# Kernel optimization log

Measured on AMD Instinct MI355X. Metric: run time of the kernel, lower is better.

Reference implementation:

```python
import jax, jax.numpy as jnp
import numpy as np

BS, NC, BH, BW, C = 1, 6, 100, 100, 256
HG, WG = 100, 40
HF, WF = 48, 80
HEADS, PTS, HD = 8, 8, 32
MAXOV = 2
NQ = HG * WG


def _nearest_sample(img, grid):
    # img: [B,H,W,Ch], grid: [B,Hg,Wg,2] in [-1,1]; nearest, align_corners=True, zeros padding
    B, H, W, _ = img.shape
    ix = jnp.round((grid[..., 0] + 1.0) * 0.5 * (W - 1))
    iy = jnp.round((grid[..., 1] + 1.0) * 0.5 * (H - 1))
    valid = (ix >= 0) & (ix <= W - 1) & (iy >= 0) & (iy <= H - 1)
    xc = jnp.clip(ix, 0, W - 1).astype(jnp.int32)
    yc = jnp.clip(iy, 0, H - 1).astype(jnp.int32)
    b = jnp.arange(B)[:, None, None]
    return img[b, yc, xc] * valid[..., None]


def _bilinear_sample(img, x, y):
    # img: [B,H,W,Ch]; x,y: [B,N] unnormalized (align_corners=False); zeros padding
    B, H, W, _ = img.shape
    x0 = jnp.floor(x)
    y0 = jnp.floor(y)
    wx1 = x - x0
    wy1 = y - y0
    b = jnp.arange(B)[:, None]

    def corner(xi, yi):
        valid = (xi >= 0) & (xi <= W - 1) & (yi >= 0) & (yi <= H - 1)
        xc = jnp.clip(xi, 0, W - 1).astype(jnp.int32)
        yc = jnp.clip(yi, 0, H - 1).astype(jnp.int32)
        return img[b, yc, xc] * valid[..., None]

    return (corner(x0, y0) * ((1 - wx1) * (1 - wy1))[..., None]
            + corner(x0 + 1, y0) * (wx1 * (1 - wy1))[..., None]
            + corner(x0, y0 + 1) * ((1 - wx1) * wy1)[..., None]
            + corner(x0 + 1, y0 + 1) * (wx1 * wy1)[..., None])


def _forward(query, value, queries_rebatch_grid, restore_bev_grid,
             reference_points_rebatch, bev_pillar_counts, query_pos,
             Wv, bv, Woff, boff, Watt, batt, Wout, bout, spatial_shapes):
    inp_residual = query
    q = query + query_pos                                       # [BS, BH*BW, C]
    # --- rebatch BEV queries per camera via nearest grid_sample ---
    qmap = jnp.broadcast_to(q.reshape(BS, 1, BH, BW, C),
                            (BS, NC, BH, BW, C)).reshape(BS * NC, BH, BW, C)
    q_reb = _nearest_sample(qmap, queries_rebatch_grid).reshape(BS * NC, NQ, C)
    ref = reference_points_rebatch.reshape(BS * NC, NQ, 2)      # flatten(-2): [BNC,NQ,2,1]->[BNC,NQ,2]
    # --- value projection ---
    v = value.transpose(2, 0, 1, 3).reshape(BS * NC, HF * WF, C)
    v = (v @ Wv + bv).reshape(BS * NC, HF, WF, HEADS, HD)
    # --- multi-scale deformable attention (single level) ---
    off = (q_reb @ Woff + boff).reshape(BS * NC, NQ, HEADS, PTS, 2)
    attw = jax.nn.softmax((q_reb @ Watt + batt).reshape(BS * NC, NQ, HEADS, PTS), axis=-1)
    normalizer = jnp.flip(spatial_shapes[0], 0).astype(jnp.float32)  # [WF, HF]
    loc = ref[:, :, None, None, :] + off / normalizer           # [BNC,NQ,HEADS,PTS,2] in [0,1]
    x = (loc[..., 0] * WF - 0.5).transpose(0, 2, 1, 3).reshape(BS * NC * HEADS, NQ * PTS)
    y = (loc[..., 1] * HF - 0.5).transpose(0, 2, 1, 3).reshape(BS * NC * HEADS, NQ * PTS)
    vh = v.transpose(0, 3, 1, 2, 4).reshape(BS * NC * HEADS, HF, WF, HD)
    samp = _bilinear_sample(vh, x, y).reshape(BS * NC, HEADS, NQ, PTS, HD)
    out = jnp.einsum('bhnpd,bnhp->bnhd', samp, attw).reshape(BS * NC, NQ, C)
    queries_out = out.transpose(0, 2, 1)                        # [BNC, C, NQ] (channels-first as module expects)
    # --- restore to BEV feature ---
    qo = queries_out.reshape(BS, NC, C, NQ).transpose(0, 2, 1, 3).reshape(BS, C, NC * HG, WG)
    bevq = _nearest_sample(qo.transpose(0, 2, 3, 1), restore_bev_grid)  # [BS, MAXOV*BH, BW, C]
    bevq = bevq.transpose(0, 3, 1, 2)                           # [BS, C, MAXOV*BH, BW]
    # reshape(BS, C*MAXOV, BH, BW) + all-ones grouped 1x1 conv == sum of the two overlap copies
    slots = bevq[:, :, :BH, :] + bevq[:, :, BH:, :]             # [BS, C, BH, BW]
    slots = slots.reshape(BS, C, BH * BW).transpose(0, 2, 1)    # [BS, BH*BW, C]
    slots = slots * bev_pillar_counts
    slots = slots @ Wout + bout
    return slots + inp_residual  # dropout identity in eval


def setup_inputs():
    key = jax.random.key(0)
    ks = jax.random.split(key, 14)
    s = 1.0 / np.sqrt(C)
    return {
        "query": jax.random.normal(ks[0], (BS, BH * BW, C), jnp.float32),
        "value": jax.random.normal(ks[1], (BS, HF * WF, NC, C), jnp.float32),
        "queries_rebatch_grid": jax.random.uniform(ks[2], (BS * NC, HG, WG, 2), jnp.float32, -1.0, 1.0),
        "restore_bev_grid": jax.random.uniform(ks[3], (BS, MAXOV * BH, BW, 2), jnp.float32, -1.0, 1.0),
        "reference_points_rebatch": jax.random.uniform(ks[4], (BS * NC, NQ, 2, 1), jnp.float32),
        "bev_pillar_counts": jax.random.uniform(ks[5], (BS, BH * BW, 1), jnp.float32),
        "query_pos": jax.random.normal(ks[6], (BS, BH * BW, C), jnp.float32),
        "Wv": jax.random.uniform(ks[7], (C, C), jnp.float32, -s, s),
        "bv": jnp.zeros((C,), jnp.float32),
        "Woff": jax.random.normal(ks[8], (C, HEADS * PTS * 2), jnp.float32) * 0.01,
        "boff": jax.random.uniform(ks[9], (HEADS * PTS * 2,), jnp.float32, -2.0, 2.0),
        "Watt": jax.random.normal(ks[10], (C, HEADS * PTS), jnp.float32) * 0.01,
        "batt": jnp.zeros((HEADS * PTS,), jnp.float32),
        "Wout": jax.random.uniform(ks[11], (C, C), jnp.float32, -s, s),
        "bout": jnp.zeros((C,), jnp.float32),
        "spatial_shapes": jnp.array([[HF, WF]], dtype=jnp.int32),
    }


def reference(query, value, queries_rebatch_grid, restore_bev_grid,
              reference_points_rebatch, bev_pillar_counts, query_pos,
              Wv, bv, Woff, boff, Watt, batt, Wout, bout, spatial_shapes):
    return _forward(query, value, queries_rebatch_grid, restore_bev_grid,
                    reference_points_rebatch, bev_pillar_counts, query_pos,
                    Wv, bv, Woff, boff, Watt, batt, Wout, bout, spatial_shapes)
```

## Files before the change

kernel.cpp:

```cpp
#include <hip/hip_runtime.h>
#include <hip/hip_bf16.h>
#include <math.h>

#define NCAMS 6
#define BH_ 100
#define BW_ 100
#define CDIM 256
#define NQ_ 4000
#define HF_ 48
#define WF_ 80
#define HEADS_ 8
#define PTS_ 8
#define HD_ 32
#define HWV (HF_*WF_)
#define M1_ (NCAMS*HWV)
#define M2_ (NCAMS*NQ_)
#define NOUT_ 10000

#define SA 264

typedef __bf16 bf16_t;
typedef __bf16 bf16x8 __attribute__((ext_vector_type(8)));
typedef __bf16 bf16x4 __attribute__((ext_vector_type(4)));
typedef float  f32x4  __attribute__((ext_vector_type(4)));

static __device__ __forceinline__ f32x4 mfma16(bf16x8 a, bf16x8 b, f32x4 c) {
    return __builtin_amdgcn_mfma_f32_16x16x32_bf16(a, b, c, 0, 0, 0);
}

__global__ __launch_bounds__(256) void k0_prep(const float* __restrict__ Wv,
                                               const float* __restrict__ Woff,
                                               const float* __restrict__ Watt,
                                               const float* __restrict__ Wout,
                                               bf16_t* __restrict__ WvT,
                                               bf16_t* __restrict__ WcombT,
                                               bf16_t* __restrict__ WoutT) {
    int b = blockIdx.x, k = threadIdx.x;
    if (b < 256) {
        WvT[b * 256 + k] = (bf16_t)Wv[k * 256 + b];
    } else if (b < 448) {
        int n = b - 256;
        float v = (n < 128) ? Woff[k * 128 + n] : Watt[k * 64 + (n - 128)];
        WcombT[n * 256 + k] = (bf16_t)v;
    } else {
        int n = b - 448;
        WoutT[n * 256 + k] = (bf16_t)Wout[k * 256 + n];
    }
}

__global__ __launch_bounds__(256) void k1_vproj(const float* __restrict__ value,
                                                const bf16_t* __restrict__ WvT,
                                                const float* __restrict__ bv,
                                                bf16_t* __restrict__ vh) {
    __shared__ __align__(16) bf16_t At[32 * SA];
    const int m0 = blockIdx.x * 32;
    const int cam = m0 / HWV;
    const int hw0 = m0 - cam * HWV;
    for (int idx = threadIdx.x; idx < 32 * 64; idx += 256) {
        int r = idx >> 6, c4 = idx & 63;
        float4 v = ((const float4*)value)[((hw0 + r) * NCAMS + cam) * 64 + c4];
        bf16x4 pk; pk[0] = (bf16_t)v.x; pk[1] = (bf16_t)v.y; pk[2] = (bf16_t)v.z; pk[3] = (bf16_t)v.w;
        *(bf16x4*)(At + r * SA + c4 * 4) = pk;
    }
    __syncthreads();
    const int lane = threadIdx.x & 63, w = threadIdx.x >> 6;
    const int lr = lane & 15, lk = lane >> 4;
    f32x4 acc[2][4] = {};
    const bf16_t* a0 = At + lr * SA + lk * 8;
    const bf16_t* b0 = WvT + (w * 64 + lr) * 256 + lk * 8;
#pragma unroll
    for (int ks = 0; ks < 8; ++ks) {
        bf16x8 af[2], bf_[4];
#pragma unroll
        for (int m = 0; m < 2; ++m) af[m] = *(const bf16x8*)(a0 + m * 16 * SA + ks * 32);
#pragma unroll
        for (int n = 0; n < 4; ++n) bf_[n] = *(const bf16x8*)(b0 + n * 16 * 256 + ks * 32);
#pragma unroll
        for (int m = 0; m < 2; ++m)
#pragma unroll
            for (int n = 0; n < 4; ++n)
                acc[m][n] = mfma16(af[m], bf_[n], acc[m][n]);
    }
    __syncthreads();
#pragma unroll
    for (int n = 0; n < 4; ++n) {
        int col = w * 64 + n * 16 + lr;
        float bias = bv[col];
#pragma unroll
        for (int m = 0; m < 2; ++m)
#pragma unroll
            for (int j = 0; j < 4; ++j)
                At[(m * 16 + lk * 4 + j) * SA + col] = (bf16_t)(acc[m][n][j] + bias);
    }
    __syncthreads();
    for (int idx = threadIdx.x; idx < 32 * 32; idx += 256) {
        int r = idx >> 5, g = idx & 31;
        int head = g >> 2, part = g & 3;
        bf16x8 v = *(const bf16x8*)(At + r * SA + g * 8);
        *(bf16x8*)(vh + ((size_t)(cam * HEADS_ + head) * HWV + hw0 + r) * HD_ + part * 8) = v;
    }
}

__global__ __launch_bounds__(256) void k2_offatt(const float* __restrict__ query,
                                                 const float* __restrict__ qpos,
                                                 const float* __restrict__ qgrid,
                                                 const bf16_t* __restrict__ WcombT,
                                                 const float* __restrict__ boff,
                                                 const float* __restrict__ batt,
                                                 float* __restrict__ off_ws,
                                                 float* __restrict__ att_ws) {
    __shared__ __align__(16) bf16_t At[32 * SA];
    __shared__ int rowpos[32];
    const int m0 = blockIdx.x * 32;
    if (threadIdx.x < 32) {
        int m = m0 + threadIdx.x;
        float gx = qgrid[m * 2 + 0], gy = qgrid[m * 2 + 1];
        float fx = rintf(__fmul_rn(__fmul_rn(__fadd_rn(gx, 1.0f), 0.5f), 99.0f));
        float fy = rintf(__fmul_rn(__fmul_rn(__fadd_rn(gy, 1.0f), 0.5f), 99.0f));
        bool valid = (fx >= 0.0f) && (fx <= 99.0f) && (fy >= 0.0f) && (fy <= 99.0f);
        rowpos[threadIdx.x] = valid ? ((int)fy * BW_ + (int)fx) : -1;
    }
    __syncthreads();
    const float4* q4 = (const float4*)query;
    const float4* p4 = (const float4*)qpos;
    for (int idx = threadIdx.x; idx < 32 * 64; idx += 256) {
        int r = idx >> 6, c4 = idx & 63;
        int p = rowpos[r];
        bf16x4 pk;
        if (p >= 0) {
            float4 a = q4[p * 64 + c4];
            float4 b = p4[p * 64 + c4];
            pk[0] = (bf16_t)(a.x + b.x); pk[1] = (bf16_t)(a.y + b.y);
            pk[2] = (bf16_t)(a.z + b.z); pk[3] = (bf16_t)(a.w + b.w);
        } else {
            pk[0] = (bf16_t)0.0f; pk[1] = (bf16_t)0.0f; pk[2] = (bf16_t)0.0f; pk[3] = (bf16_t)0.0f;
        }
        *(bf16x4*)(At + r * SA + c4 * 4) = pk;
    }
    __syncthreads();
    const int lane = threadIdx.x & 63, w = threadIdx.x >> 6;
    const int lr = lane & 15, lk = lane >> 4;
    const int wcol0 = w * 48;
    f32x4 acc[2][3] = {};
    const bf16_t* a0 = At + lr * SA + lk * 8;
    const bf16_t* b0 = WcombT + (wcol0 + lr) * 256 + lk * 8;
#pragma unroll
    for (int ks = 0; ks < 8; ++ks) {
        bf16x8 af[2], bf_[3];
#pragma unroll
        for (int m = 0; m < 2; ++m) af[m] = *(const bf16x8*)(a0 + m * 16 * SA + ks * 32);
#pragma unroll
        for (int n = 0; n < 3; ++n) bf_[n] = *(const bf16x8*)(b0 + n * 16 * 256 + ks * 32);
#pragma unroll
        for (int m = 0; m < 2; ++m)
#pragma unroll
            for (int n = 0; n < 3; ++n)
                acc[m][n] = mfma16(af[m], bf_[n], acc[m][n]);
    }
#pragma unroll
    for (int n = 0; n < 3; ++n) {
        const int colbase = wcol0 + n * 16;
        const int col = colbase + lr;
        if (colbase < 128) {
            float bo = boff[col];
#pragma unroll
            for (int m = 0; m < 2; ++m)
#pragma unroll
                for (int j = 0; j < 4; ++j)
                    off_ws[(m0 + m * 16 + lk * 4 + j) * 128 + col] = acc[m][n][j] + bo;
        } else {
            float bt = batt[col - 128];
#pragma unroll
            for (int m = 0; m < 2; ++m)
#pragma unroll
                for (int j = 0; j < 4; ++j) {
                    float lg = acc[m][n][j] + bt;
                    float mx = lg;
                    mx = fmaxf(mx, __shfl_xor(mx, 1, 64));
                    mx = fmaxf(mx, __shfl_xor(mx, 2, 64));
                    mx = fmaxf(mx, __shfl_xor(mx, 4, 64));
                    float e = expf(lg - mx);
                    float s = e;
                    s += __shfl_xor(s, 1, 64);
                    s += __shfl_xor(s, 2, 64);
                    s += __shfl_xor(s, 4, 64);
                    att_ws[(m0 + m * 16 + lk * 4 + j) * 64 + (col - 128)] = e / s;
                }
        }
    }
}

__global__ __launch_bounds__(256) void k3_sample(const bf16_t* __restrict__ vh,
                                                 const float* __restrict__ refp,
                                                 const float* __restrict__ off_ws,
                                                 const float* __restrict__ att_ws,
                                                 bf16_t* __restrict__ out_attn) {
    const int lb = (blockIdx.x & 7) * 375 + (blockIdx.x >> 3);
    const int t = lb * 256 + threadIdx.x;
    const int u = t >> 2;
    const int j = t & 3;
    const int m = u >> 3;
    const int h = u & 7;
    const int cam = m / NQ_;
    const float rx = refp[m * 2 + 0];
    const float ry = refp[m * 2 + 1];
    const bf16_t* base = vh + (size_t)(cam * HEADS_ + h) * HWV * HD_ + j * 8;
    const float4* off4 = (const float4*)(off_ws + m * 128 + h * 16);
    const float4* att4 = (const float4*)(att_ws + m * 64 + h * 8);
    float4 o0 = off4[0], o1 = off4[1], o2 = off4[2], o3 = off4[3];
    float4 a0 = att4[0], a1 = att4[1];
    float offv[16] = {o0.x, o0.y, o0.z, o0.w, o1.x, o1.y, o1.z, o1.w,
                      o2.x, o2.y, o2.z, o2.w, o3.x, o3.y, o3.z, o3.w};
    float attv[8] = {a0.x, a0.y, a0.z, a0.w, a1.x, a1.y, a1.z, a1.w};
    float acc[8] = {};
#pragma unroll
    for (int p = 0; p < PTS_; ++p) {
        float ax = fmaf(rx, (float)WF_, offv[p * 2 + 0] - 0.5f);
        float ay = fmaf(ry, (float)HF_, offv[p * 2 + 1] - 0.5f);
        float x0f = floorf(ax), y0f = floorf(ay);
        float wx = ax - x0f, wy = ay - y0f;
        float att = attv[p];
        bool vx0 = (x0f >= 0.0f) && (x0f <= (float)(WF_ - 1));
        bool vx1 = (x0f >= -1.0f) && (x0f <= (float)(WF_ - 2));
        bool vy0 = (y0f >= 0.0f) && (y0f <= (float)(HF_ - 1));
        bool vy1 = (y0f >= -1.0f) && (y0f <= (float)(HF_ - 2));
        float aw00 = (vx0 && vy0) ? att * (1.0f - wx) * (1.0f - wy) : 0.0f;
        float aw01 = (vx1 && vy0) ? att * wx * (1.0f - wy) : 0.0f;
        float aw10 = (vx0 && vy1) ? att * (1.0f - wx) * wy : 0.0f;
        float aw11 = (vx1 && vy1) ? att * wx * wy : 0.0f;
        int x0 = (int)fminf(fmaxf(x0f, 0.0f), (float)(WF_ - 1));
        int x1 = (int)fminf(fmaxf(x0f + 1.0f, 0.0f), (float)(WF_ - 1));
        int y0 = (int)fminf(fmaxf(y0f, 0.0f), (float)(HF_ - 1));
        int y1 = (int)fminf(fmaxf(y0f + 1.0f, 0.0f), (float)(HF_ - 1));
        bf16x8 c00 = *(const bf16x8*)(base + (y0 * WF_ + x0) * HD_);
        bf16x8 c01 = *(const bf16x8*)(base + (y0 * WF_ + x1) * HD_);
        bf16x8 c10 = *(const bf16x8*)(base + (y1 * WF_ + x0) * HD_);
        bf16x8 c11 = *(const bf16x8*)(base + (y1 * WF_ + x1) * HD_);
#pragma unroll
        for (int c = 0; c < 8; ++c) {
            acc[c] = fmaf(aw00, (float)c00[c],
                     fmaf(aw01, (float)c01[c],
                     fmaf(aw10, (float)c10[c],
                     fmaf(aw11, (float)c11[c], acc[c]))));
        }
    }
    bf16x8 ov;
#pragma unroll
    for (int c = 0; c < 8; ++c) ov[c] = (bf16_t)acc[c];
    *(bf16x8*)(out_attn + (size_t)m * CDIM + h * HD_ + j * 8) = ov;
}

__global__ __launch_bounds__(256) void k4_restore(const bf16_t* __restrict__ out_attn,
                                                  const float* __restrict__ rgrid,
                                                  const float* __restrict__ counts,
                                                  const bf16_t* __restrict__ WoutT,
                                                  const float* __restrict__ bout,
                                                  const float* __restrict__ query,
                                                  float* __restrict__ out) {
    __shared__ __align__(16) bf16_t At[32 * SA];
    __shared__ int pos2[32][2];
    __shared__ float cnt[32];
    const int m0 = blockIdx.x * 32;
    if (threadIdx.x < 64) {
        int r = threadIdx.x >> 1, k = threadIdx.x & 1;
        int i = m0 + r;
        if (i < NOUT_) {
            int bh = i / 100, bw = i - bh * 100;
            int R = bh + k * BH_;
            float gx = rgrid[(R * 100 + bw) * 2 + 0], gy = rgrid[(R * 100 + bw) * 2 + 1];
            float fx = rintf(__fmul_rn(__fmul_rn(__fadd_rn(gx, 1.0f), 0.5f), 39.0f));
            float fy = rintf(__fmul_rn(__fmul_rn(__fadd_rn(gy, 1.0f), 0.5f), 599.0f));
            bool valid = (fx >= 0.0f) && (fx <= 39.0f) && (fy >= 0.0f) && (fy <= 599.0f);
            int ix = (int)fx, iy = (int)fy;
            int camr = iy / 100, hg = iy - camr * 100;
            pos2[r][k] = valid ? (camr * NQ_ + hg * 40 + ix) : -1;
            if (k == 0) cnt[r] = counts[i];
        } else {
            pos2[r][k] = -1;
            if (k == 0) cnt[r] = 0.0f;
        }
    }
    __syncthreads();
    for (int idx = threadIdx.x; idx < 32 * 32; idx += 256) {
        int r = idx >> 5, g = idx & 31;
        int p0 = pos2[r][0], p1 = pos2[r][1];
        float s[8] = {};
        if (p0 >= 0) {
            bf16x8 a = *(const bf16x8*)(out_attn + (size_t)p0 * CDIM + g * 8);
#pragma unroll
            for (int c = 0; c < 8; ++c) s[c] += (float)a[c];
        }
        if (p1 >= 0) {
            bf16x8 a = *(const bf16x8*)(out_attn + (size_t)p1 * CDIM + g * 8);
#pragma unroll
            for (int c = 0; c < 8; ++c) s[c] += (float)a[c];
        }
        float cn = cnt[r];
        bf16x8 pk;
#pragma unroll
        for (int c = 0; c < 8; ++c) pk[c] = (bf16_t)(s[c] * cn);
        *(bf16x8*)(At + r * SA + g * 8) = pk;
    }
    __syncthreads();
    const int lane = threadIdx.x & 63, w = threadIdx.x >> 6;
    const int lr = lane & 15, lk = lane >> 4;
    f32x4 acc[2][4] = {};
    const bf16_t* a0 = At + lr * SA + lk * 8;
    const bf16_t* b0 = WoutT + (w * 64 + lr) * 256 + lk * 8;
#pragma unroll
    for (int ks = 0; ks < 8; ++ks) {
        bf16x8 af[2], bf_[4];
#pragma unroll
        for (int m = 0; m < 2; ++m) af[m] = *(const bf16x8*)(a0 + m * 16 * SA + ks * 32);
#pragma unroll
        for (int n = 0; n < 4; ++n) bf_[n] = *(const bf16x8*)(b0 + n * 16 * 256 + ks * 32);
#pragma unroll
        for (int m = 0; m < 2; ++m)
#pragma unroll
            for (int n = 0; n < 4; ++n)
                acc[m][n] = mfma16(af[m], bf_[n], acc[m][n]);
    }
#pragma unroll
    for (int n = 0; n < 4; ++n) {
        int col = w * 64 + n * 16 + lr;
        float bo = bout[col];
#pragma unroll
        for (int m = 0; m < 2; ++m)
#pragma unroll
            for (int j = 0; j < 4; ++j) {
                int row = m0 + m * 16 + lk * 4 + j;
                if (row < NOUT_)
                    out[row * CDIM + col] = acc[m][n][j] + bo + query[row * CDIM + col];
            }
    }
}

extern "C" void kernel_launch(void* const* d_in, const int* in_sizes, int n_in,
                              void* d_out, int out_size, void* d_ws, size_t ws_size,
                              hipStream_t stream) {
    (void)in_sizes; (void)n_in; (void)out_size; (void)ws_size;
    const float* query  = (const float*)d_in[0];
    const float* value  = (const float*)d_in[1];
    const float* qgrid  = (const float*)d_in[2];
    const float* rgrid  = (const float*)d_in[3];
    const float* refp   = (const float*)d_in[4];
    const float* counts = (const float*)d_in[5];
    const float* qpos   = (const float*)d_in[6];
    const float* Wv     = (const float*)d_in[7];
    const float* bv     = (const float*)d_in[8];
    const float* Woff   = (const float*)d_in[9];
    const float* boff   = (const float*)d_in[10];
    const float* Watt   = (const float*)d_in[11];
    const float* batt   = (const float*)d_in[12];
    const float* Wout   = (const float*)d_in[13];
    const float* bout   = (const float*)d_in[14];
    float* out = (float*)d_out;
    char* w8 = (char*)d_ws;

    bf16_t* vh       = (bf16_t*)(w8);
    bf16_t* out_attn = (bf16_t*)(w8 + 11796480);
    float* off_ws    = (float*)(w8 + 24084480);
    float* att_ws    = (float*)(w8 + 36372480);
    bf16_t* WvT      = (bf16_t*)(w8 + 42516480);
    bf16_t* WcombT   = (bf16_t*)(w8 + 42647552);
    bf16_t* WoutT    = (bf16_t*)(w8 + 42745856);

    hipLaunchKernelGGL(k0_prep,   dim3(704),      dim3(256), 0, stream, Wv, Woff, Watt, Wout,
                       WvT, WcombT, WoutT);
    hipLaunchKernelGGL(k1_vproj,  dim3(M1_ / 32), dim3(256), 0, stream, value, WvT, bv, vh);
    hipLaunchKernelGGL(k2_offatt, dim3(M2_ / 32), dim3(256), 0, stream, query, qpos, qgrid,
                       WcombT, boff, batt, off_ws, att_ws);
    hipLaunchKernelGGL(k3_sample, dim3(3000),     dim3(256), 0, stream, vh, refp, off_ws,
                       att_ws, out_attn);
    hipLaunchKernelGGL(k4_restore, dim3(313),     dim3(256), 0, stream, out_attn, rgrid, counts,
                       WoutT, bout, query, out);
}
```

Measured before the change: 97.65 us.

## Fuse offset/attention projection with deformable sampling, keeping offsets in LDS

Merges the offset/attention GEMM kernel and the bilinear sampling kernel into one kernel. Each block handles 16 query rows, writes offsets and softmaxed attention weights to shared memory instead of global workspace, then samples the value map directly. This removes a launch and the global round trip of about 18 MB of fp32 offsets and weights. In exchange the GEMM tile shrinks to 16 rows, so each block reloads weight fragments for half as much work, and the block index is remapped so that consecutive row tiles stay on the same XCD.

Result: faster. 95.25 us (-2.5%).

```diff
diff --git a/kernel.cpp b/kernel.cpp
--- a/kernel.cpp
+++ b/kernel.cpp
@@ -18,6 +18,8 @@
 #define NOUT_ 10000
 
 #define SA 264
+#define SOFF 132
+#define SATT 68
 
 typedef __bf16 bf16_t;
 typedef __bf16 bf16x8 __attribute__((ext_vector_type(8)));
@@ -72,14 +74,14 @@
     for (int ks = 0; ks < 8; ++ks) {
         bf16x8 af[2], bf_[4];
 #pragma unroll
-        for (int m = 0; m < 2; ++m) af[m] = *(const bf16x8*)(a0 + m * 16 * SA + ks * 32);
+        for (int mm = 0; mm < 2; ++mm) af[mm] = *(const bf16x8*)(a0 + mm * 16 * SA + ks * 32);
 #pragma unroll
         for (int n = 0; n < 4; ++n) bf_[n] = *(const bf16x8*)(b0 + n * 16 * 256 + ks * 32);
 #pragma unroll
-        for (int m = 0; m < 2; ++m)
+        for (int mm = 0; mm < 2; ++mm)
 #pragma unroll
             for (int n = 0; n < 4; ++n)
-                acc[m][n] = mfma16(af[m], bf_[n], acc[m][n]);
+                acc[mm][n] = mfma16(af[mm], bf_[n], acc[mm][n]);
     }
     __syncthreads();
 #pragma unroll
@@ -87,10 +89,10 @@
         int col = w * 64 + n * 16 + lr;
         float bias = bv[col];
 #pragma unroll
-        for (int m = 0; m < 2; ++m)
+        for (int mm = 0; mm < 2; ++mm)
 #pragma unroll
             for (int j = 0; j < 4; ++j)
-                At[(m * 16 + lk * 4 + j) * SA + col] = (bf16_t)(acc[m][n][j] + bias);
+                At[(mm * 16 + lk * 4 + j) * SA + col] = (bf16_t)(acc[mm][n][j] + bias);
     }
     __syncthreads();
     for (int idx = threadIdx.x; idx < 32 * 32; idx += 256) {
@@ -101,153 +103,163 @@
     }
 }
 
-__global__ __launch_bounds__(256) void k2_offatt(const float* __restrict__ query,
-                                                 const float* __restrict__ qpos,
-                                                 const float* __restrict__ qgrid,
-                                                 const bf16_t* __restrict__ WcombT,
-                                                 const float* __restrict__ boff,
-                                                 const float* __restrict__ batt,
-                                                 float* __restrict__ off_ws,
-                                                 float* __restrict__ att_ws) {
-    __shared__ __align__(16) bf16_t At[32 * SA];
-    __shared__ int rowpos[32];
-    const int m0 = blockIdx.x * 32;
-    if (threadIdx.x < 32) {
+__global__ __launch_bounds__(256) void k23_offatt_sample(
+        const float* __restrict__ query,
+        const float* __restrict__ qpos,
+        const float* __restrict__ qgrid,
+        const bf16_t* __restrict__ WcombT,
+        const float* __restrict__ boff,
+        const float* __restrict__ batt,
+        const float* __restrict__ refp,
+        const bf16_t* __restrict__ vh,
+        bf16_t* __restrict__ out_attn) {
+    __shared__ __align__(16) char u_lds[16 * SOFF * 4 + 16 * SATT * 4];
+    bf16_t* At   = (bf16_t*)u_lds;
+    float*  offs = (float*)u_lds;
+    float*  atts = (float*)(u_lds + 16 * SOFF * 4);
+    __shared__ int rowpos[16];
+    __shared__ float rref[16][2];
+
+    const int orig = blockIdx.x;
+    const int xcd = orig & 7, idx8 = orig >> 3;
+    const int lb = (xcd < 4 ? xcd * 188 : 4 * 188 + (xcd - 4) * 187) + idx8;
+    const int m0 = lb * 16;
+    const int cam = m0 / NQ_;
+
+    if (threadIdx.x < 16) {
         int m = m0 + threadIdx.x;
         float gx = qgrid[m * 2 + 0], gy = qgrid[m * 2 + 1];
         float fx = rintf(__fmul_rn(__fmul_rn(__fadd_rn(gx, 1.0f), 0.5f), 99.0f));
         float fy = rintf(__fmul_rn(__fmul_rn(__fadd_rn(gy, 1.0f), 0.5f), 99.0f));
         bool valid = (fx >= 0.0f) && (fx <= 99.0f) && (fy >= 0.0f) && (fy <= 99.0f);
         rowpos[threadIdx.x] = valid ? ((int)fy * BW_ + (int)fx) : -1;
+    } else if (threadIdx.x < 48) {
+        int t = threadIdx.x - 16;
+        rref[t >> 1][t & 1] = refp[(m0 + (t >> 1)) * 2 + (t & 1)];
     }
     __syncthreads();
     const float4* q4 = (const float4*)query;
     const float4* p4 = (const float4*)qpos;
-    for (int idx = threadIdx.x; idx < 32 * 64; idx += 256) {
-        int r = idx >> 6, c4 = idx & 63;
-        int p = rowpos[r];
-        bf16x4 pk;
-        if (p >= 0) {
-            float4 a = q4[p * 64 + c4];
-            float4 b = p4[p * 64 + c4];
-            pk[0] = (bf16_t)(a.x + b.x); pk[1] = (bf16_t)(a.y + b.y);
-            pk[2] = (bf16_t)(a.z + b.z); pk[3] = (bf16_t)(a.w + b.w);
-        } else {
-            pk[0] = (bf16_t)0.0f; pk[1] = (bf16_t)0.0f; pk[2] = (bf16_t)0.0f; pk[3] = (bf16_t)0.0f;
-        }
-        *(bf16x4*)(At + r * SA + c4 * 4) = pk;
+    {
+        int idx = threadIdx.x;
+#pragma unroll
+        for (int it = 0; it < 4; ++it, idx += 256) {
+            int r = idx >> 6, c4 = idx & 63;
+            int p = rowpos[r];
+            bf16x4 pk;
+            if (p >= 0) {
+                float4 a = q4[p * 64 + c4];
+                float4 b = p4[p * 64 + c4];
+                pk[0] = (bf16_t)(a.x + b.x); pk[1] = (bf16_t)(a.y + b.y);
+                pk[2] = (bf16_t)(a.z + b.z); pk[3] = (bf16_t)(a.w + b.w);
+            } else {
+                pk[0] = (bf16_t)0.0f; pk[1] = (bf16_t)0.0f; pk[2] = (bf16_t)0.0f; pk[3] = (bf16_t)0.0f;
+            }
+            *(bf16x4*)(At + r * SA + c4 * 4) = pk;
+        }
     }
     __syncthreads();
     const int lane = threadIdx.x & 63, w = threadIdx.x >> 6;
     const int lr = lane & 15, lk = lane >> 4;
     const int wcol0 = w * 48;
-    f32x4 acc[2][3] = {};
-    const bf16_t* a0 = At + lr * SA + lk * 8;
-    const bf16_t* b0 = WcombT + (wcol0 + lr) * 256 + lk * 8;
-#pragma unroll
-    for (int ks = 0; ks < 8; ++ks) {
-        bf16x8 af[2], bf_[3];
-#pragma unroll
-        for (int m = 0; m < 2; ++m) af[m] = *(const bf16x8*)(a0 + m * 16 * SA + ks * 32);
-#pragma unroll
-        for (int n = 0; n < 3; ++n) bf_[n] = *(const bf16x8*)(b0 + n * 16 * 256 + ks * 32);
-#pragma unroll
-        for (int m = 0; m < 2; ++m)
+    f32x4 acc[3] = {};
+    {
+        const bf16_t* a0 = At + lr * SA + lk * 8;
+        const bf16_t* b0 = WcombT + (wcol0 + lr) * 256 + lk * 8;
+#pragma unroll
+        for (int ks = 0; ks < 8; ++ks) {
+            bf16x8 af = *(const bf16x8*)(a0 + ks * 32);
+            bf16x8 bf_[3];
+#pragma unroll
+            for (int n = 0; n < 3; ++n) bf_[n] = *(const bf16x8*)(b0 + n * 16 * 256 + ks * 32);
 #pragma unroll
             for (int n = 0; n < 3; ++n)
-                acc[m][n] = mfma16(af[m], bf_[n], acc[m][n]);
-    }
+                acc[n] = mfma16(af, bf_[n], acc[n]);
+        }
+    }
+    __syncthreads();
 #pragma unroll
     for (int n = 0; n < 3; ++n) {
         const int colbase = wcol0 + n * 16;
         const int col = colbase + lr;
+        const int rloc = lk * 4;
         if (colbase < 128) {
             float bo = boff[col];
 #pragma unroll
-            for (int m = 0; m < 2; ++m)
-#pragma unroll
-                for (int j = 0; j < 4; ++j)
-                    off_ws[(m0 + m * 16 + lk * 4 + j) * 128 + col] = acc[m][n][j] + bo;
+            for (int j = 0; j < 4; ++j)
+                offs[(rloc + j) * SOFF + col] = acc[n][j] + bo;
         } else {
             float bt = batt[col - 128];
 #pragma unroll
-            for (int m = 0; m < 2; ++m)
-#pragma unroll
-                for (int j = 0; j < 4; ++j) {
-                    float lg = acc[m][n][j] + bt;
-                    float mx = lg;
-                    mx = fmaxf(mx, __shfl_xor(mx, 1, 64));
-                    mx = fmaxf(mx, __shfl_xor(mx, 2, 64));
-                    mx = fmaxf(mx, __shfl_xor(mx, 4, 64));
-                    float e = expf(lg - mx);
-                    float s = e;
-                    s += __shfl_xor(s, 1, 64);
-                    s += __shfl_xor(s, 2, 64);
-                    s += __shfl_xor(s, 4, 64);
-                    att_ws[(m0 + m * 16 + lk * 4 + j) * 64 + (col - 128)] = e / s;
-                }
-        }
-    }
-}
-
-__global__ __launch_bounds__(256) void k3_sample(const bf16_t* __restrict__ vh,
-                                                 const float* __restrict__ refp,
-                                                 const float* __restrict__ off_ws,
-                                                 const float* __restrict__ att_ws,
-                                                 bf16_t* __restrict__ out_attn) {
-    const int lb = (blockIdx.x & 7) * 375 + (blockIdx.x >> 3);
-    const int t = lb * 256 + threadIdx.x;
-    const int u = t >> 2;
-    const int j = t & 3;
-    const int m = u >> 3;
-    const int h = u & 7;
-    const int cam = m / NQ_;
-    const float rx = refp[m * 2 + 0];
-    const float ry = refp[m * 2 + 1];
-    const bf16_t* base = vh + (size_t)(cam * HEADS_ + h) * HWV * HD_ + j * 8;
-    const float4* off4 = (const float4*)(off_ws + m * 128 + h * 16);
-    const float4* att4 = (const float4*)(att_ws + m * 64 + h * 8);
-    float4 o0 = off4[0], o1 = off4[1], o2 = off4[2], o3 = off4[3];
-    float4 a0 = att4[0], a1 = att4[1];
-    float offv[16] = {o0.x, o0.y, o0.z, o0.w, o1.x, o1.y, o1.z, o1.w,
-                      o2.x, o2.y, o2.z, o2.w, o3.x, o3.y, o3.z, o3.w};
-    float attv[8] = {a0.x, a0.y, a0.z, a0.w, a1.x, a1.y, a1.z, a1.w};
-    float acc[8] = {};
-#pragma unroll
-    for (int p = 0; p < PTS_; ++p) {
-        float ax = fmaf(rx, (float)WF_, offv[p * 2 + 0] - 0.5f);
-        float ay = fmaf(ry, (float)HF_, offv[p * 2 + 1] - 0.5f);
-        float x0f = floorf(ax), y0f = floorf(ay);
-        float wx = ax - x0f, wy = ay - y0f;
-        float att = attv[p];
-        bool vx0 = (x0f >= 0.0f) && (x0f <= (float)(WF_ - 1));
-        bool vx1 = (x0f >= -1.0f) && (x0f <= (float)(WF_ - 2));
-        bool vy0 = (y0f >= 0.0f) && (y0f <= (float)(HF_ - 1));
-        bool vy1 = (y0f >= -1.0f) && (y0f <= (float)(HF_ - 2));
-        float aw00 = (vx0 && vy0) ? att * (1.0f - wx) * (1.0f - wy) : 0.0f;
-        float aw01 = (vx1 && vy0) ? att * wx * (1.0f - wy) : 0.0f;
-        float aw10 = (vx0 && vy1) ? att * (1.0f - wx) * wy : 0.0f;
-        float aw11 = (vx1 && vy1) ? att * wx * wy : 0.0f;
-        int x0 = (int)fminf(fmaxf(x0f, 0.0f), (float)(WF_ - 1));
-        int x1 = (int)fminf(fmaxf(x0f + 1.0f, 0.0f), (float)(WF_ - 1));
-        int y0 = (int)fminf(fmaxf(y0f, 0.0f), (float)(HF_ - 1));
-        int y1 = (int)fminf(fmaxf(y0f + 1.0f, 0.0f), (float)(HF_ - 1));
-        bf16x8 c00 = *(const bf16x8*)(base + (y0 * WF_ + x0) * HD_);
-        bf16x8 c01 = *(const bf16x8*)(base + (y0 * WF_ + x1) * HD_);
-        bf16x8 c10 = *(const bf16x8*)(base + (y1 * WF_ + x0) * HD_);
-        bf16x8 c11 = *(const bf16x8*)(base + (y1 * WF_ + x1) * HD_);
-#pragma unroll
-        for (int c = 0; c < 8; ++c) {
-            acc[c] = fmaf(aw00, (float)c00[c],
-                     fmaf(aw01, (float)c01[c],
-                     fmaf(aw10, (float)c10[c],
-                     fmaf(aw11, (float)c11[c], acc[c]))));
-        }
-    }
-    bf16x8 ov;
-#pragma unroll
-    for (int c = 0; c < 8; ++c) ov[c] = (bf16_t)acc[c];
-    *(bf16x8*)(out_attn + (size_t)m * CDIM + h * HD_ + j * 8) = ov;
+            for (int j = 0; j < 4; ++j) {
+                float lg = acc[n][j] + bt;
+                float mx = lg;
+                mx = fmaxf(mx, __shfl_xor(mx, 1, 64));
+                mx = fmaxf(mx, __shfl_xor(mx, 2, 64));
+                mx = fmaxf(mx, __shfl_xor(mx, 4, 64));
+                float e = expf(lg - mx);
+                float s = e;
+                s += __shfl_xor(s, 1, 64);
+                s += __shfl_xor(s, 2, 64);
+                s += __shfl_xor(s, 4, 64);
+                atts[(rloc + j) * SATT + (col - 128)] = e / s;
+            }
+        }
+    }
+    __syncthreads();
+    const int j = threadIdx.x & 3;
+#pragma unroll
+    for (int rep = 0; rep < 2; ++rep) {
+        const int unit = rep * 64 + (threadIdx.x >> 2);
+        const int r = unit >> 3, h = unit & 7;
+        const int m = m0 + r;
+        const float rx = rref[r][0];
+        const float ry = rref[r][1];
+        const bf16_t* base = vh + (size_t)(cam * HEADS_ + h) * HWV * HD_ + j * 8;
+        const float4* off4 = (const float4*)(offs + r * SOFF + h * 16);
+        const float4* att4 = (const float4*)(atts + r * SATT + h * 8);
+        float4 o0 = off4[0], o1 = off4[1], o2 = off4[2], o3 = off4[3];
+        float4 a0 = att4[0], a1 = att4[1];
+        float offv[16] = {o0.x, o0.y, o0.z, o0.w, o1.x, o1.y, o1.z, o1.w,
+                          o2.x, o2.y, o2.z, o2.w, o3.x, o3.y, o3.z, o3.w};
+        float attv[8] = {a0.x, a0.y, a0.z, a0.w, a1.x, a1.y, a1.z, a1.w};
+        float acc2[8] = {};
+#pragma unroll
+        for (int p = 0; p < PTS_; ++p) {
+            float ax = fmaf(rx, (float)WF_, offv[p * 2 + 0] - 0.5f);
+            float ay = fmaf(ry, (float)HF_, offv[p * 2 + 1] - 0.5f);
+            float x0f = floorf(ax), y0f = floorf(ay);
+            float wx = ax - x0f, wy = ay - y0f;
+            float att = attv[p];
+            bool vx0 = (x0f >= 0.0f) && (x0f <= (float)(WF_ - 1));
+            bool vx1 = (x0f >= -1.0f) && (x0f <= (float)(WF_ - 2));
+            bool vy0 = (y0f >= 0.0f) && (y0f <= (float)(HF_ - 1));
+            bool vy1 = (y0f >= -1.0f) && (y0f <= (float)(HF_ - 2));
+            float aw00 = (vx0 && vy0) ? att * (1.0f - wx) * (1.0f - wy) : 0.0f;
+            float aw01 = (vx1 && vy0) ? att * wx * (1.0f - wy) : 0.0f;
+            float aw10 = (vx0 && vy1) ? att * (1.0f - wx) * wy : 0.0f;
+            float aw11 = (vx1 && vy1) ? att * wx * wy : 0.0f;
+            int x0 = (int)fminf(fmaxf(x0f, 0.0f), (float)(WF_ - 1));
+            int x1 = (int)fminf(fmaxf(x0f + 1.0f, 0.0f), (float)(WF_ - 1));
+            int y0 = (int)fminf(fmaxf(y0f, 0.0f), (float)(HF_ - 1));
+            int y1 = (int)fminf(fmaxf(y0f + 1.0f, 0.0f), (float)(HF_ - 1));
+            bf16x8 c00 = *(const bf16x8*)(base + (y0 * WF_ + x0) * HD_);
+            bf16x8 c01 = *(const bf16x8*)(base + (y0 * WF_ + x1) * HD_);
+            bf16x8 c10 = *(const bf16x8*)(base + (y1 * WF_ + x0) * HD_);
+            bf16x8 c11 = *(const bf16x8*)(base + (y1 * WF_ + x1) * HD_);
+#pragma unroll
+            for (int c = 0; c < 8; ++c) {
+                acc2[c] = fmaf(aw00, (float)c00[c],
+                          fmaf(aw01, (float)c01[c],
+                          fmaf(aw10, (float)c10[c],
+                          fmaf(aw11, (float)c11[c], acc2[c]))));
+            }
+        }
+        bf16x8 ov;
+#pragma unroll
+        for (int c = 0; c < 8; ++c) ov[c] = (bf16_t)acc2[c];
+        *(bf16x8*)(out_attn + (size_t)m * CDIM + h * HD_ + j * 8) = ov;
+    }
 }
 
 __global__ __launch_bounds__(256) void k4_restore(const bf16_t* __restrict__ out_attn,
@@ -311,26 +323,26 @@
     for (int ks = 0; ks < 8; ++ks) {
         bf16x8 af[2], bf_[4];
 #pragma unroll
-        for (int m = 0; m < 2; ++m) af[m] = *(const bf16x8*)(a0 + m * 16 * SA + ks * 32);
+        for (int mm = 0; mm < 2; ++mm) af[mm] = *(const bf16x8*)(a0 + mm * 16 * SA + ks * 32);
 #pragma unroll
         for (int n = 0; n < 4; ++n) bf_[n] = *(const bf16x8*)(b0 + n * 16 * 256 + ks * 32);
 #pragma unroll
-        for (int m = 0; m < 2; ++m)
+        for (int mm = 0; mm < 2; ++mm)
 #pragma unroll
             for (int n = 0; n < 4; ++n)
-                acc[m][n] = mfma16(af[m], bf_[n], acc[m][n]);
+                acc[mm][n] = mfma16(af[mm], bf_[n], acc[mm][n]);
     }
 #pragma unroll
     for (int n = 0; n < 4; ++n) {
         int col = w * 64 + n * 16 + lr;
         float bo = bout[col];
 #pragma unroll
-        for (int m = 0; m < 2; ++m)
+        for (int mm = 0; mm < 2; ++mm)
 #pragma unroll
             for (int j = 0; j < 4; ++j) {
-                int row = m0 + m * 16 + lk * 4 + j;
+                int row = m0 + mm * 16 + lk * 4 + j;
                 if (row < NOUT_)
-                    out[row * CDIM + col] = acc[m][n][j] + bo + query[row * CDIM + col];
+                    out[row * CDIM + col] = acc[mm][n][j] + bo + query[row * CDIM + col];
             }
     }
 }
@@ -359,19 +371,15 @@
 
     bf16_t* vh       = (bf16_t*)(w8);
     bf16_t* out_attn = (bf16_t*)(w8 + 11796480);
-    float* off_ws    = (float*)(w8 + 24084480);
-    float* att_ws    = (float*)(w8 + 36372480);
-    bf16_t* WvT      = (bf16_t*)(w8 + 42516480);
-    bf16_t* WcombT   = (bf16_t*)(w8 + 42647552);
-    bf16_t* WoutT    = (bf16_t*)(w8 + 42745856);
+    bf16_t* WvT      = (bf16_t*)(w8 + 24084480);
+    bf16_t* WcombT   = (bf16_t*)(w8 + 24215552);
+    bf16_t* WoutT    = (bf16_t*)(w8 + 24313856);
 
     hipLaunchKernelGGL(k0_prep,   dim3(704),      dim3(256), 0, stream, Wv, Woff, Watt, Wout,
                        WvT, WcombT, WoutT);
     hipLaunchKernelGGL(k1_vproj,  dim3(M1_ / 32), dim3(256), 0, stream, value, WvT, bv, vh);
-    hipLaunchKernelGGL(k2_offatt, dim3(M2_ / 32), dim3(256), 0, stream, query, qpos, qgrid,
-                       WcombT, boff, batt, off_ws, att_ws);
-    hipLaunchKernelGGL(k3_sample, dim3(3000),     dim3(256), 0, stream, vh, refp, off_ws,
-                       att_ws, out_attn);
+    hipLaunchKernelGGL(k23_offatt_sample, dim3(M2_ / 16), dim3(256), 0, stream,
+                       query, qpos, qgrid, WcombT, boff, batt, refp, vh, out_attn);
     hipLaunchKernelGGL(k4_restore, dim3(313),     dim3(256), 0, stream, out_attn, rgrid, counts,
                        WoutT, bout, query, out);
 }
```
